# Optimization experiments

Hardware: AMD Instinct MI355X
Metric: run time of the kernel (lower is better)

Reference implementation:

```python
import jax, jax.numpy as jnp
import numpy as np

NHEAD = 8
LAYER_NAMES = ('self', 'cross', 'self', 'cross')
EPS = 1e-6


def ln(x, g, b, eps=1e-5):
    m = jnp.mean(x, -1, keepdims=True)
    v = jnp.mean((x - m) ** 2, -1, keepdims=True)
    return (x - m) * jax.lax.rsqrt(v + eps) * g + b


def linear_attention(q, k, v, q_mask, kv_mask):
    # q: [N, L, H, D], k/v: [N, S, H, D]; LoFTR LinearAttention (elu+1 feature map)
    Q = jax.nn.elu(q) + 1.0
    K = jax.nn.elu(k) + 1.0
    if q_mask is not None:
        Q = Q * q_mask[:, :, None, None].astype(Q.dtype)
    if kv_mask is not None:
        mk = kv_mask[:, :, None, None].astype(K.dtype)
        K = K * mk
        v = v * mk
    v_len = v.shape[1]
    v = v / v_len
    KV = jnp.einsum('nshd,nshv->nhdv', K, v)
    Z = 1.0 / (jnp.einsum('nlhd,nhd->nlh', Q, K.sum(1)) + EPS)
    return jnp.einsum('nlhd,nhdv,nlh->nlhv', Q, KV, Z) * v_len


def enc_layer(x, src, q_mask, kv_mask, Wq, Wk, Wv, Wm, W1, W2, g1, b1, g2, b2):
    # x: [N, L, C], src: [N, S, C]
    N, L, C = x.shape
    S = src.shape[1]
    H, D = NHEAD, C // NHEAD
    q = (x @ Wq).reshape(N, L, H, D)
    k = (src @ Wk).reshape(N, S, H, D)
    v = (src @ Wv).reshape(N, S, H, D)
    msg = linear_attention(q, k, v, q_mask, kv_mask).reshape(N, L, C)
    msg = ln(msg @ Wm, g1, b1)
    msg = ln(jnp.tanh(jnp.concatenate([x, msg], axis=-1) @ W1) @ W2, g2, b2)
    return x + msg


def sample_descriptors(kp, fmap, s):
    # kp: [B, L, K, 2] (x, y) raw-image pixel coords; fmap: [B, C, H, W]; s: stride
    B, C, H, W = fmap.shape
    k = kp - s / 2 + 0.5
    denom = jnp.array([W * s - s / 2 - 0.5, H * s - s / 2 - 0.5], dtype=kp.dtype)
    k = (k / denom) * 2.0 - 1.0  # normalized [-1, 1]
    px = (k[..., 0] + 1.0) * 0.5 * (W - 1)  # align_corners=True grid_sample
    py = (k[..., 1] + 1.0) * 0.5 * (H - 1)
    x0 = jnp.floor(px)
    y0 = jnp.floor(py)
    wx = (px - x0)[..., None]
    wy = (py - y0)[..., None]
    x0i = jnp.clip(x0, 0, W - 1).astype(jnp.int32)
    x1i = jnp.clip(x0 + 1, 0, W - 1).astype(jnp.int32)
    y0i = jnp.clip(y0, 0, H - 1).astype(jnp.int32)
    y1i = jnp.clip(y0 + 1, 0, H - 1).astype(jnp.int32)
    fm = jnp.transpose(fmap, (0, 2, 3, 1))  # [B, H, W, C]
    bidx = jnp.arange(B)[:, None, None]
    g00 = fm[bidx, y0i, x0i]
    g01 = fm[bidx, y0i, x1i]
    g10 = fm[bidx, y1i, x0i]
    g11 = fm[bidx, y1i, x1i]
    out = (1 - wy) * ((1 - wx) * g00 + wx * g01) + wy * ((1 - wx) * g10 + wx * g11)
    # SuperPoint-style L2 normalization of sampled descriptors
    out = out / (jnp.linalg.norm(out, axis=-1, keepdims=True) + 1e-8)
    return out  # [B, L, K, C]


def geo_transformer(feat0, feat1, kp0_cross, kp1_cross, mask_self0, mask_self1,
                    mask_cross0, mask_cross1, Wq, Wk, Wv, Wm, W1, W2, g1, b1, g2, b2,
                    h0, w0, h1, w1, scale):
    B, L0, C = feat0.shape
    L1 = feat1.shape[1]
    K = kp0_cross.shape[2]
    for i, name in enumerate(LAYER_NAMES):
        p = (Wq[i], Wk[i], Wv[i], Wm[i], W1[i], W2[i], g1[i], b1[i], g2[i], b2[i])
        if name == 'self':
            # source = masked subset of x == full source with kv-mask (v_length cancels)
            feat0 = enc_layer(feat0, feat0, None, mask_self0, *p)
            feat1 = enc_layer(feat1, feat1, None, mask_self1, *p)
        else:
            fmap0 = jnp.transpose(feat0.reshape(B, h0, w0, C), (0, 3, 1, 2))
            fmap1 = jnp.transpose(feat1.reshape(B, h1, w1, C), (0, 3, 1, 2))
            f0c = sample_descriptors(kp0_cross, fmap0, scale)  # [B, L1, K, C]
            f1c = sample_descriptors(kp1_cross, fmap1, scale)  # [B, L0, K, C]
            x0 = feat0.reshape(B * L0, 1, C)
            x1 = feat1.reshape(B * L1, 1, C)
            nf0 = enc_layer(x0, f1c.reshape(B * L0, K, C), None,
                            mask_cross1.reshape(B * L0, K), *p)
            nf1 = enc_layer(x1, f0c.reshape(B * L1, K, C), None,
                            mask_cross0.reshape(B * L1, K), *p)
            feat0 = nf0.reshape(B, L0, C)
            feat1 = nf1.reshape(B, L1, C)
    return feat0, feat1


def setup_inputs() -> dict:
    key = jax.random.key(0)
    B, H0, W0, C, K, S, NL = 2, 64, 64, 256, 9, 8, 4
    L = H0 * W0
    ks = jax.random.split(key, 16)
    std = (2.0 / (C + C)) ** 0.5
    std2 = (2.0 / (2 * C + 2 * C)) ** 0.5
    std3 = (2.0 / (2 * C + C)) ** 0.5
    kp0 = jnp.stack([
        jax.random.uniform(ks[2], (B, L, K)) * (W0 * S),
        jax.random.uniform(ks[3], (B, L, K)) * (H0 * S)], axis=-1)
    kp1 = jnp.stack([
        jax.random.uniform(ks[4], (B, L, K)) * (W0 * S),
        jax.random.uniform(ks[5], (B, L, K)) * (H0 * S)], axis=-1)
    return {
        'feat0': jax.random.normal(ks[0], (B, L, C), jnp.float32),
        'feat1': jax.random.normal(ks[1], (B, L, C), jnp.float32),
        'kp0_cross': kp0.astype(jnp.float32),
        'kp1_cross': kp1.astype(jnp.float32),
        'mask_self0': jax.random.bernoulli(ks[6], 0.9, (B, L)),
        'mask_self1': jax.random.bernoulli(ks[7], 0.9, (B, L)),
        'mask_cross0': jax.random.bernoulli(ks[8], 0.8, (B, L, K)),
        'mask_cross1': jax.random.bernoulli(ks[9], 0.8, (B, L, K)),
        'Wq': jax.random.normal(ks[10], (NL, C, C), jnp.float32) * std,
        'Wk': jax.random.normal(ks[11], (NL, C, C), jnp.float32) * std,
        'Wv': jax.random.normal(ks[12], (NL, C, C), jnp.float32) * std,
        'Wm': jax.random.normal(ks[13], (NL, C, C), jnp.float32) * std,
        'W1': jax.random.normal(ks[14], (NL, 2 * C, 2 * C), jnp.float32) * std2,
        'W2': jax.random.normal(ks[15], (NL, 2 * C, C), jnp.float32) * std3,
        'g1': jnp.ones((NL, C), jnp.float32),
        'b1': jnp.zeros((NL, C), jnp.float32),
        'g2': jnp.ones((NL, C), jnp.float32),
        'b2': jnp.zeros((NL, C), jnp.float32),
        'h0': H0, 'w0': W0, 'h1': H0, 'w1': W0, 'scale': S,
    }


def reference(feat0, feat1, kp0_cross, kp1_cross, mask_self0, mask_self1,
              mask_cross0, mask_cross1, Wq, Wk, Wv, Wm, W1, W2, g1, b1, g2, b2,
              h0, w0, h1, w1, scale):
    return geo_transformer(feat0, feat1, kp0_cross, kp1_cross, mask_self0, mask_self1,
                           mask_cross0, mask_cross1, Wq, Wk, Wv, Wm, W1, W2,
                           g1, b1, g2, b2, h0, w0, h1, w1, scale)
```

## Files before the change

kernel.cpp:

```cpp
#include <hip/hip_runtime.h>
#include <cstddef>


#define NROWS 16384

typedef unsigned short ushort_t;
typedef __attribute__((ext_vector_type(8))) short short8;
typedef __attribute__((ext_vector_type(4))) float f32x4;
typedef __attribute__((ext_vector_type(4))) unsigned short ushort4_t;
typedef __attribute__((ext_vector_type(8))) unsigned short ushort8_t;

__device__ __forceinline__ float b2f(unsigned short u) {
    union { unsigned int i; float f; } v; v.i = (unsigned int)u << 16; return v.f;
}
__device__ __forceinline__ unsigned short f2b(float x) {
    union { float f; unsigned int i; } v; v.f = x;
    unsigned int r = v.i + 0x7fffu + ((v.i >> 16) & 1u);
    return (unsigned short)(r >> 16);
}
__device__ __forceinline__ float elu1(float x) {
    return x > 0.f ? x + 1.f : __expf(x);
}

#define ASYNC_COPY16(gptr, lptr) \
    __builtin_amdgcn_global_load_lds((const __attribute__((address_space(1))) void*)(gptr), \
                                     (__attribute__((address_space(3))) void*)(lptr), 16, 0, 0)

template<int ACT>
__global__ __launch_bounds__(256) void gemm_bf16_kernel(
    const ushort_t* __restrict__ A0, const ushort_t* __restrict__ A1, int ksplit,
    int lda0, int lda1, const ushort_t* __restrict__ Wt, int ldw,
    ushort_t* __restrict__ C, int ldc, int Kd)
{
    __shared__ ushort_t As[128 * 64];
    __shared__ ushort_t Bs[128 * 64];

    int tid = threadIdx.x;
    int m0 = blockIdx.y * 128;
    int n0 = blockIdx.x * 128;
    int lane = tid & 63, w = tid >> 6;
    int wrow = w >> 1, wcol = w & 1;
    int quad = lane >> 4, l16 = lane & 15;

    f32x4 acc[4][4];
    #pragma unroll
    for (int i = 0; i < 4; i++)
        #pragma unroll
        for (int j = 0; j < 4; j++) acc[i][j] = (f32x4){0.f, 0.f, 0.f, 0.f};

    for (int kb = 0; kb < Kd; kb += 64) {
        const ushort_t* Ab; int lda, kc;
        if (kb < ksplit) { Ab = A0; lda = lda0; kc = kb; }
        else             { Ab = A1; lda = lda1; kc = kb - ksplit; }

        #pragma unroll
        for (int q = 0; q < 4; q++) {
            int s = q * 256 + tid;
            int kk = s >> 9, p = s & 511;
            int row = p >> 2, c4 = p & 3;
            ASYNC_COPY16(Ab + (size_t)(m0 + row) * lda + kc + kk * 32 + c4 * 8,
                         (char*)As + s * 16);
        }
        #pragma unroll
        for (int q = 0; q < 4; q++) {
            int s = q * 256 + tid;
            int kk = s >> 9, p = s & 511;
            int row = p >> 2, c4 = p & 3;
            ASYNC_COPY16(Wt + (size_t)(n0 + row) * ldw + kb + kk * 32 + c4 * 8,
                         (char*)Bs + s * 16);
        }
        __syncthreads();

        #pragma unroll
        for (int kk = 0; kk < 2; kk++) {
            short8 af[4], bf[4];
            #pragma unroll
            for (int mt = 0; mt < 4; mt++)
                af[mt] = *(const short8*)&As[kk * 4096 + (wrow * 64 + mt * 16 + l16) * 32 + quad * 8];
            #pragma unroll
            for (int nt = 0; nt < 4; nt++)
                bf[nt] = *(const short8*)&Bs[kk * 4096 + (wcol * 64 + nt * 16 + l16) * 32 + quad * 8];
            #pragma unroll
            for (int mt = 0; mt < 4; mt++)
                #pragma unroll
                for (int nt = 0; nt < 4; nt++)
                    acc[mt][nt] = __builtin_amdgcn_mfma_f32_16x16x32_bf16(
                        af[mt], bf[nt], acc[mt][nt], 0, 0, 0);
        }
        __syncthreads();
    }

    #pragma unroll
    for (int mt = 0; mt < 4; mt++) {
        int row = m0 + wrow * 64 + mt * 16 + quad * 4;
        #pragma unroll
        for (int nt = 0; nt < 4; nt++) {
            int col = n0 + wcol * 64 + nt * 16 + l16;
            #pragma unroll
            for (int r = 0; r < 4; r++) {
                float v = acc[mt][nt][r];
                if (ACT) v = tanhf(v);
                C[(size_t)(row + r) * ldc + col] = f2b(v);
            }
        }
    }
}

template<int RES>
__global__ __launch_bounds__(256) void gemm_ln_kernel(
    const ushort_t* __restrict__ A, int lda,
    const ushort_t* __restrict__ Wt, int ldw, int Kd,
    const float* __restrict__ g, const float* __restrict__ bp,
    ushort_t* __restrict__ OutBf,
    const float* __restrict__ Xin, float* __restrict__ Xout)
{
    __shared__ ushort_t As[32 * 64];
    __shared__ ushort_t Bs[256 * 64];
    __shared__ float rsum[4][32];
    __shared__ float rsq[4][32];

    int tid = threadIdx.x;
    int m0 = blockIdx.x * 32;
    int lane = tid & 63, w = tid >> 6;
    int quad = lane >> 4, l16 = lane & 15;

    f32x4 acc[2][4];
    #pragma unroll
    for (int i = 0; i < 2; i++)
        #pragma unroll
        for (int j = 0; j < 4; j++) acc[i][j] = (f32x4){0.f, 0.f, 0.f, 0.f};

    for (int kb = 0; kb < Kd; kb += 64) {
        {
            int s = tid;
            int kk = s >> 7, p = s & 127;
            int row = p >> 2, c4 = p & 3;
            ASYNC_COPY16(A + (size_t)(m0 + row) * lda + kb + kk * 32 + c4 * 8,
                         (char*)As + s * 16);
        }
        #pragma unroll
        for (int q = 0; q < 8; q++) {
            int s = q * 256 + tid;
            int kk = s >> 10, p = s & 1023;
            int row = p >> 2, c4 = p & 3;
            ASYNC_COPY16(Wt + (size_t)(row) * ldw + kb + kk * 32 + c4 * 8,
                         (char*)Bs + s * 16);
        }
        __syncthreads();

        #pragma unroll
        for (int kk = 0; kk < 2; kk++) {
            short8 af[2], bf[4];
            #pragma unroll
            for (int mt = 0; mt < 2; mt++)
                af[mt] = *(const short8*)&As[kk * 1024 + (mt * 16 + l16) * 32 + quad * 8];
            #pragma unroll
            for (int nt = 0; nt < 4; nt++)
                bf[nt] = *(const short8*)&Bs[kk * 8192 + (w * 64 + nt * 16 + l16) * 32 + quad * 8];
            #pragma unroll
            for (int mt = 0; mt < 2; mt++)
                #pragma unroll
                for (int nt = 0; nt < 4; nt++)
                    acc[mt][nt] = __builtin_amdgcn_mfma_f32_16x16x32_bf16(
                        af[mt], bf[nt], acc[mt][nt], 0, 0, 0);
        }
        __syncthreads();
    }

    #pragma unroll
    for (int mt = 0; mt < 2; mt++)
        #pragma unroll
        for (int r = 0; r < 4; r++) {
            float s = 0.f, q = 0.f;
            #pragma unroll
            for (int nt = 0; nt < 4; nt++) {
                float v = acc[mt][nt][r];
                s += v; q += v * v;
            }
            #pragma unroll
            for (int off = 1; off < 16; off <<= 1) {
                s += __shfl_xor(s, off, 64);
                q += __shfl_xor(q, off, 64);
            }
            if (l16 == 0) {
                rsum[w][mt * 16 + quad * 4 + r] = s;
                rsq[w][mt * 16 + quad * 4 + r]  = q;
            }
        }
    __syncthreads();

    #pragma unroll
    for (int mt = 0; mt < 2; mt++) {
        #pragma unroll
        for (int r = 0; r < 4; r++) {
            int rl = mt * 16 + quad * 4 + r;
            float s = rsum[0][rl] + rsum[1][rl] + rsum[2][rl] + rsum[3][rl];
            float q = rsq[0][rl] + rsq[1][rl] + rsq[2][rl] + rsq[3][rl];
            float m = s * (1.f / 256.f);
            float var = q * (1.f / 256.f) - m * m;
            float rs = rsqrtf(var + 1e-5f);
            size_t row = (size_t)(m0 + rl);
            #pragma unroll
            for (int nt = 0; nt < 4; nt++) {
                int col = w * 64 + nt * 16 + l16;
                float y = (acc[mt][nt][r] - m) * rs * g[col] + bp[col];
                if (RES) {
                    float xn = Xin[row * 256 + col] + y;
                    Xout[row * 256 + col] = xn;
                    OutBf[row * 256 + col] = f2b(xn);
                } else {
                    OutBf[row * 256 + col] = f2b(y);
                }
            }
        }
    }
}

__global__ __launch_bounds__(256) void wprep_kernel(
    const float* __restrict__ Wq, const float* __restrict__ Wk,
    const float* __restrict__ Wv, const float* __restrict__ Wm,
    const float* __restrict__ W1, const float* __restrict__ W2,
    ushort_t* __restrict__ Wqkvt, ushort_t* __restrict__ Wmt,
    ushort_t* __restrict__ W1t, ushort_t* __restrict__ W2t)
{
    int t = blockIdx.x;
    int layer = t / 640, r = t % 640;
    const float* src; ushort_t* dst;
    int ldsrc, lddst, tn, tk;
    if (r < 192) {
        int grp = r / 64, rr = r % 64; tn = rr / 8; tk = rr % 8;
        src = (grp == 0 ? Wq : grp == 1 ? Wk : Wv) + (size_t)layer * 65536;
        ldsrc = 256;
        dst = Wqkvt + (size_t)layer * 196608 + (size_t)grp * 65536;
        lddst = 256;
    } else if (r < 256) {
        int rr = r - 192; tn = rr / 8; tk = rr % 8;
        src = Wm + (size_t)layer * 65536; ldsrc = 256;
        dst = Wmt + (size_t)layer * 65536; lddst = 256;
    } else if (r < 512) {
        int rr = r - 256; tn = rr / 16; tk = rr % 16;
        src = W1 + (size_t)layer * 262144; ldsrc = 512;
        dst = W1t + (size_t)layer * 262144; lddst = 512;
    } else {
        int rr = r - 512; tn = rr / 16; tk = rr % 16;
        src = W2 + (size_t)layer * 131072; ldsrc = 256;
        dst = W2t + (size_t)layer * 131072; lddst = 512;
    }
    int n0 = tn * 32, k0 = tk * 32;
    __shared__ float tileS[32][33];
    int j = threadIdx.x & 31, i0 = threadIdx.x >> 5;
    #pragma unroll
    for (int p = 0; p < 4; p++) {
        int i = i0 + p * 8;
        tileS[i][j] = src[(size_t)(k0 + i) * ldsrc + n0 + j];
    }
    __syncthreads();
    #pragma unroll
    for (int p = 0; p < 4; p++) {
        int i = i0 + p * 8;
        dst[(size_t)(n0 + i) * lddst + k0 + j] = f2b(tileS[j][i]);
    }
}

__global__ __launch_bounds__(256) void init_kernel(
    const float* __restrict__ f0, const float* __restrict__ f1,
    float* __restrict__ X, ushort_t* __restrict__ Xbf)
{
    int idx = blockIdx.x * 256 + threadIdx.x;
    size_t e = (size_t)idx * 4;
    float4 v = (e < 2097152) ? *(const float4*)&f0[e] : *(const float4*)&f1[e - 2097152];
    *(float4*)&X[e] = v;
    ushort4_t u = { f2b(v.x), f2b(v.y), f2b(v.z), f2b(v.w) };
    *(ushort4_t*)&Xbf[e] = u;
}

__global__ __launch_bounds__(256) void kv_reduce_kernel(
    const ushort_t* __restrict__ QKV,
    const int* __restrict__ mask0, const int* __restrict__ mask1,
    float* __restrict__ KV, float* __restrict__ Ksum)
{
    int g = blockIdx.y;
    int t = g >> 4, b = (g >> 3) & 1, h = g & 7;
    const int* mask = t ? mask1 : mask0;
    int rowbase = t * 8192 + b * 4096;
    int s_begin = blockIdx.x * 256;

    __shared__ float sK[32][32];
    __shared__ float sV[32][32];

    int tid = threadIdx.x;
    int e  = tid & 31;
    int dq = tid >> 5;

    float acc[4] = {0.f, 0.f, 0.f, 0.f};
    float ks[4]  = {0.f, 0.f, 0.f, 0.f};

    for (int s0 = s_begin; s0 < s_begin + 256; s0 += 32) {
        #pragma unroll
        for (int q = 0; q < 2; q++) {
            int idx = tid + q * 256;
            int rl = idx >> 4;
            int part = idx & 15;
            int s = s0 + rl;
            size_t row = (size_t)(rowbase + s);
            float m = mask[b * 4096 + s] ? 1.f : 0.f;
            if (part < 8) {
                ushort4_t u = *(const ushort4_t*)&QKV[row * 768 + 256 + h * 32 + part * 4];
                float4 f = { elu1(b2f(u.x)) * m, elu1(b2f(u.y)) * m,
                             elu1(b2f(u.z)) * m, elu1(b2f(u.w)) * m };
                *(float4*)&sK[rl][part * 4] = f;
            } else {
                ushort4_t u = *(const ushort4_t*)&QKV[row * 768 + 512 + h * 32 + (part - 8) * 4];
                float4 f = { b2f(u.x) * m, b2f(u.y) * m, b2f(u.z) * m, b2f(u.w) * m };
                *(float4*)&sV[rl][(part - 8) * 4] = f;
            }
        }
        __syncthreads();

        #pragma unroll
        for (int s = 0; s < 32; s++) {
            float4 kq = *(const float4*)&sK[s][dq * 4];
            float vv = sV[s][e];
            acc[0] += kq.x * vv;
            acc[1] += kq.y * vv;
            acc[2] += kq.z * vv;
            acc[3] += kq.w * vv;
            ks[0] += kq.x; ks[1] += kq.y; ks[2] += kq.z; ks[3] += kq.w;
        }
        __syncthreads();
    }

    #pragma unroll
    for (int j = 0; j < 4; j++)
        atomicAdd(&KV[(size_t)g * 1024 + (dq * 4 + j) * 32 + e], acc[j]);
    if (e == 0) {
        #pragma unroll
        for (int j = 0; j < 4; j++)
            atomicAdd(&Ksum[g * 32 + dq * 4 + j], ks[j]);
    }
}

__global__ __launch_bounds__(256) void attn_apply_kernel(
    const ushort_t* __restrict__ QKV, const float* __restrict__ KV,
    const float* __restrict__ Ksum, ushort_t* __restrict__ MSG)
{
    int row = blockIdx.x;
    int t = row >> 13, bb = (row >> 12) & 1;
    int gb = (t * 2 + bb) * 8;
    int c = threadIdx.x, h = c >> 5, e = c & 31;
    int g = gb + h;

    __shared__ float sQ[256];
    float qf = elu1(b2f(QKV[(size_t)row * 768 + c]));
    sQ[c] = qf;
    __syncthreads();

    float p = qf * Ksum[g * 32 + e];
    #pragma unroll
    for (int off = 16; off; off >>= 1) p += __shfl_xor(p, off, 32);
    float Z = 1.f / (p + 1e-6f);

    float acc = 0.f;
    #pragma unroll
    for (int d = 0; d < 32; d++)
        acc += sQ[h * 32 + d] * KV[(size_t)g * 1024 + d * 32 + e];

    MSG[(size_t)row * 256 + c] = f2b(acc * Z);
}

__global__ __launch_bounds__(256) void gram_kernel(
    const ushort_t* __restrict__ Xbf, float* __restrict__ Gm)
{
    int a = blockIdx.x * 4 + (threadIdx.x >> 6);
    int lane = threadIdx.x & 63;
    int img = a / 4225;
    int rr = a - img * 4225;
    int ay = rr / 65, ax = rr - ay * 65;
    int xa = ax > 0 ? ax - 1 : 0;
    int xb = ax < 64 ? ax : 63;
    if (ax == 0) xb = 0;
    int ya = ay > 0 ? ay - 1 : 0;
    int yb = ay < 64 ? ay : 63;
    if (ay == 0) yb = 0;

    size_t rbase = (size_t)img * 4096;
    size_t r0 = (rbase + ya * 64 + xa) * 256;
    size_t r1 = (rbase + ya * 64 + xb) * 256;
    size_t r2 = (rbase + yb * 64 + xa) * 256;
    size_t r3 = (rbase + yb * 64 + xb) * 256;

    int c4 = lane * 4;
    ushort4_t u0 = *(const ushort4_t*)&Xbf[r0 + c4];
    ushort4_t u1 = *(const ushort4_t*)&Xbf[r1 + c4];
    ushort4_t u2 = *(const ushort4_t*)&Xbf[r2 + c4];
    ushort4_t u3 = *(const ushort4_t*)&Xbf[r3 + c4];

    float p[10] = {0,0,0,0,0,0,0,0,0,0};
    #pragma unroll
    for (int j = 0; j < 4; j++) {
        float f0 = b2f(u0[j]), f1 = b2f(u1[j]), f2 = b2f(u2[j]), f3 = b2f(u3[j]);
        p[0] += f0 * f0; p[1] += f0 * f1; p[2] += f0 * f2; p[3] += f0 * f3;
        p[4] += f1 * f1; p[5] += f1 * f2; p[6] += f1 * f3;
        p[7] += f2 * f2; p[8] += f2 * f3; p[9] += f3 * f3;
    }
    #pragma unroll
    for (int k = 0; k < 10; k++)
        #pragma unroll
        for (int off = 32; off; off >>= 1) p[k] += __shfl_xor(p[k], off, 64);

    if (lane == 0) {
        #pragma unroll
        for (int k = 0; k < 10; k++) Gm[(size_t)a * 10 + k] = p[k];
    }
}

__global__ __launch_bounds__(256) void cross_fused_kernel(
    const ushort_t* __restrict__ QKV, const float* __restrict__ Gm,
    const float* __restrict__ kp0, const float* __restrict__ kp1,
    const int* __restrict__ maskc0, const int* __restrict__ maskc1,
    ushort_t* __restrict__ MSG)
{
    int wv = threadIdx.x >> 6;
    int lane = threadIdx.x & 63;
    int half = lane >> 5;
    int l32 = lane & 31;
    int row = blockIdx.x * 4 + wv;

    int t = row >> 13;
    int bl = row & 8191;
    int ts = 1 - t;
    const float* kp = ts ? kp1 : kp0;
    const int* mask = (t == 0) ? maskc1 : maskc0;
    int img = ts * 2 + (bl >> 12);
    size_t rb = (size_t)img * 4096;
    const float* Gimg = Gm + (size_t)img * 42250;

    int c8 = l32 * 8;

    ushort8_t qu = *(const ushort8_t*)&QKV[(size_t)row * 768 + c8];
    float qf[8];
    #pragma unroll
    for (int j = 0; j < 8; j++) qf[j] = elu1(b2f(qu[j]));

    float zsum = 0.f;
    float acc[8] = {0,0,0,0,0,0,0,0};

    for (int s9 = half; s9 < 9; s9 += 2) {
        int r = bl * 9 + s9;
        bool mk = mask[r] != 0;
        if (mk) {
            float xx = kp[(size_t)r * 2 + 0];
            float yy = kp[(size_t)r * 2 + 1];
            float px = (xx - 3.5f) * (63.f / 507.5f);
            float py = (yy - 3.5f) * (63.f / 507.5f);
            float fx = floorf(px), fy = floorf(py);
            float wx = px - fx, wy = py - fy;
            int ix = (int)fx, iy = (int)fy;
            int xa = ix > 0 ? ix : 0;
            int xb = ix + 1 > 0 ? (ix + 1 < 63 ? ix + 1 : 63) : 0;
            int ya = iy > 0 ? iy : 0;
            int yb = iy + 1 > 0 ? (iy + 1 < 63 ? iy + 1 : 63) : 0;

            float w0 = (1.f - wy) * (1.f - wx);
            float w1 = (1.f - wy) * wx;
            float w2 = wy * (1.f - wx);
            float w3 = wy * wx;

            const float* G = &Gimg[(size_t)((iy + 1) * 65 + (ix + 1)) * 10];
            float g00 = G[0], g01 = G[1], g02 = G[2], g03 = G[3], g11 = G[4];
            float g12 = G[5], g13 = G[6], g22 = G[7], g23 = G[8], g33 = G[9];
            float ss = w0 * w0 * g00 + w1 * w1 * g11 + w2 * w2 * g22 + w3 * w3 * g33
                     + 2.f * (w0 * w1 * g01 + w0 * w2 * g02 + w0 * w3 * g03
                            + w1 * w2 * g12 + w1 * w3 * g13 + w2 * w3 * g23);
            float inv = 1.f / (sqrtf(ss) + 1e-8f);
            float u0 = w0 * inv, u1 = w1 * inv, u2 = w2 * inv, u3 = w3 * inv;

            size_t s00 = (rb + ya * 64 + xa) * 768;
            size_t s01 = (rb + ya * 64 + xb) * 768;
            size_t s10 = (rb + yb * 64 + xa) * 768;
            size_t s11 = (rb + yb * 64 + xb) * 768;

            ushort8_t k00 = *(const ushort8_t*)&QKV[s00 + 256 + c8];
            ushort8_t k01 = *(const ushort8_t*)&QKV[s01 + 256 + c8];
            ushort8_t k10 = *(const ushort8_t*)&QKV[s10 + 256 + c8];
            ushort8_t k11 = *(const ushort8_t*)&QKV[s11 + 256 + c8];
            ushort8_t v00 = *(const ushort8_t*)&QKV[s00 + 512 + c8];
            ushort8_t v01 = *(const ushort8_t*)&QKV[s01 + 512 + c8];
            ushort8_t v10 = *(const ushort8_t*)&QKV[s10 + 512 + c8];
            ushort8_t v11 = *(const ushort8_t*)&QKV[s11 + 512 + c8];

            float vc[8];
            float p = 0.f;
            #pragma unroll
            for (int j = 0; j < 8; j++) {
                float kc = u0 * b2f(k00[j]) + u1 * b2f(k01[j])
                         + u2 * b2f(k10[j]) + u3 * b2f(k11[j]);
                vc[j] = u0 * b2f(v00[j]) + u1 * b2f(v01[j])
                      + u2 * b2f(v10[j]) + u3 * b2f(v11[j]);
                p += qf[j] * elu1(kc);
            }
            p += __shfl_xor(p, 1, 64);
            p += __shfl_xor(p, 2, 64);

            zsum += p;
            #pragma unroll
            for (int j = 0; j < 8; j++) acc[j] += p * vc[j];
        }
    }

    zsum += __shfl_xor(zsum, 32, 64);
    #pragma unroll
    for (int j = 0; j < 8; j++) acc[j] += __shfl_xor(acc[j], 32, 64);

    if (half == 0) {
        float Z = 1.f / (zsum + 1e-6f);
        ushort8_t o;
        #pragma unroll
        for (int j = 0; j < 8; j++) o[j] = f2b(acc[j] * Z);
        *(ushort8_t*)&MSG[(size_t)row * 256 + c8] = o;
    }
}


extern "C" void kernel_launch(void* const* d_in, const int* in_sizes, int n_in,
                              void* d_out, int out_size, void* d_ws, size_t ws_size,
                              hipStream_t stream)
{
    const float* feat0 = (const float*)d_in[0];
    const float* feat1 = (const float*)d_in[1];
    const float* kp0 = (const float*)d_in[2];
    const float* kp1 = (const float*)d_in[3];
    const int* ms0 = (const int*)d_in[4];
    const int* ms1 = (const int*)d_in[5];
    const int* mc0 = (const int*)d_in[6];
    const int* mc1 = (const int*)d_in[7];
    const float* Wq = (const float*)d_in[8];
    const float* Wk = (const float*)d_in[9];
    const float* Wv = (const float*)d_in[10];
    const float* Wm = (const float*)d_in[11];
    const float* W1 = (const float*)d_in[12];
    const float* W2 = (const float*)d_in[13];
    const float* g1 = (const float*)d_in[14];
    const float* b1 = (const float*)d_in[15];
    const float* g2 = (const float*)d_in[16];
    const float* b2 = (const float*)d_in[17];

    char* p = (char*)d_ws;
    float*    X     = (float*)p;            p += 16777216;
    ushort_t* Xbf   = (ushort_t*)p;         p += 8388608;
    ushort_t* QKV   = (ushort_t*)p;         p += 25165824;
    ushort_t* MSG   = (ushort_t*)p;         p += 8388608;
    ushort_t* T     = (ushort_t*)p;         p += 16777216;
    ushort_t* L1bf  = (ushort_t*)p;         p += 8388608;
    float*    KVb   = (float*)p;            p += 131072;
    float*    KSb   = (float*)p;            p += 4096;
    float*    Gm    = (float*)p;            p += 679936;
    ushort_t* Wqkvt = (ushort_t*)p;         p += 1572864;
    ushort_t* Wmt   = (ushort_t*)p;         p += 524288;
    ushort_t* W1t   = (ushort_t*)p;         p += 2097152;
    ushort_t* W2t   = (ushort_t*)p;         p += 1048576;

    init_kernel<<<4096, 256, 0, stream>>>(feat0, feat1, X, Xbf);
    wprep_kernel<<<2560, 256, 0, stream>>>(Wq, Wk, Wv, Wm, W1, W2, Wqkvt, Wmt, W1t, W2t);

    auto gemm = [&](const ushort_t* A0, const ushort_t* A1, int ksplit, int lda0, int lda1,
                    const ushort_t* Wtp, int ldw, ushort_t* Cp, int ldc, int N, int Kd, int act) {
        dim3 grid(N / 128, NROWS / 128);
        if (act)
            gemm_bf16_kernel<1><<<grid, 256, 0, stream>>>(A0, A1, ksplit, lda0, lda1, Wtp, ldw, Cp, ldc, Kd);
        else
            gemm_bf16_kernel<0><<<grid, 256, 0, stream>>>(A0, A1, ksplit, lda0, lda1, Wtp, ldw, Cp, ldc, Kd);
    };

    for (int i = 0; i < 4; i++) {
        const ushort_t* Wqkvt_l = Wqkvt + (size_t)i * 196608;
        const ushort_t* Wmt_l   = Wmt   + (size_t)i * 65536;
        const ushort_t* W1t_l   = W1t   + (size_t)i * 262144;
        const ushort_t* W2t_l   = W2t   + (size_t)i * 131072;
        const float* g1_l = g1 + (size_t)i * 256;
        const float* b1_l = b1 + (size_t)i * 256;
        const float* g2_l = g2 + (size_t)i * 256;
        const float* b2_l = b2 + (size_t)i * 256;
        bool is_self = (i == 0 || i == 2);

        gemm(Xbf, nullptr, 1 << 30, 256, 0, Wqkvt_l, 256, QKV, 768, 768, 256, 0);

        if (is_self) {
            hipMemsetAsync(KVb, 0, 33792 * 4, stream);
            kv_reduce_kernel<<<dim3(16, 32), 256, 0, stream>>>(QKV, ms0, ms1, KVb, KSb);
            attn_apply_kernel<<<NROWS, 256, 0, stream>>>(QKV, KVb, KSb, MSG);
        } else {
            gram_kernel<<<4225, 256, 0, stream>>>(Xbf, Gm);
            cross_fused_kernel<<<NROWS / 4, 256, 0, stream>>>(QKV, Gm, kp0, kp1, mc0, mc1, MSG);
        }

        gemm_ln_kernel<0><<<NROWS / 32, 256, 0, stream>>>(
            MSG, 256, Wmt_l, 256, 256, g1_l, b1_l, L1bf, nullptr, nullptr);
        gemm(Xbf, L1bf, 256, 256, 256, W1t_l, 512, T, 512, 512, 512, 1);
        float* Xout = (i == 3) ? (float*)d_out : X;
        gemm_ln_kernel<1><<<NROWS / 32, 256, 0, stream>>>(
            T, 512, W2t_l, 512, 512, g2_l, b2_l, Xbf, X, Xout);
    }
}
```

Measured before the change: 638.6 us.

## Fuse W1 tanh GEMM and W2 GEMM+LayerNorm+residual into one MLP kernel

Replaces the separate W1 GEMM (with tanh) writing the T intermediate and the W2 GEMM+LN+residual kernel with a single kernel per 32-row block. The tanh output is kept in a swizzled LDS tile instead of going through global memory. This removes a 16MB intermediate write and read plus one launch per layer. The cost is that each 32-row block re-streams the full W1 and W2 weights, which means more weight traffic and lower MFMA reuse per block, with only 512 blocks and a large LDS footprint limiting occupancy.

```diff
diff --git a/kernel.cpp b/kernel.cpp
--- a/kernel.cpp
+++ b/kernel.cpp
@@ -26,10 +26,9 @@
     __builtin_amdgcn_global_load_lds((const __attribute__((address_space(1))) void*)(gptr), \
                                      (__attribute__((address_space(3))) void*)(lptr), 16, 0, 0)
 
-template<int ACT>
 __global__ __launch_bounds__(256) void gemm_bf16_kernel(
-    const ushort_t* __restrict__ A0, const ushort_t* __restrict__ A1, int ksplit,
-    int lda0, int lda1, const ushort_t* __restrict__ Wt, int ldw,
+    const ushort_t* __restrict__ A0, int lda0,
+    const ushort_t* __restrict__ Wt, int ldw,
     ushort_t* __restrict__ C, int ldc, int Kd)
 {
     __shared__ ushort_t As[128 * 64];
@@ -49,16 +48,12 @@
         for (int j = 0; j < 4; j++) acc[i][j] = (f32x4){0.f, 0.f, 0.f, 0.f};
 
     for (int kb = 0; kb < Kd; kb += 64) {
-        const ushort_t* Ab; int lda, kc;
-        if (kb < ksplit) { Ab = A0; lda = lda0; kc = kb; }
-        else             { Ab = A1; lda = lda1; kc = kb - ksplit; }
-
         #pragma unroll
         for (int q = 0; q < 4; q++) {
             int s = q * 256 + tid;
             int kk = s >> 9, p = s & 511;
             int row = p >> 2, c4 = p & 3;
-            ASYNC_COPY16(Ab + (size_t)(m0 + row) * lda + kc + kk * 32 + c4 * 8,
+            ASYNC_COPY16(A0 + (size_t)(m0 + row) * lda0 + kb + kk * 32 + c4 * 8,
                          (char*)As + s * 16);
         }
         #pragma unroll
@@ -97,22 +92,17 @@
         for (int nt = 0; nt < 4; nt++) {
             int col = n0 + wcol * 64 + nt * 16 + l16;
             #pragma unroll
-            for (int r = 0; r < 4; r++) {
-                float v = acc[mt][nt][r];
-                if (ACT) v = tanhf(v);
-                C[(size_t)(row + r) * ldc + col] = f2b(v);
-            }
-        }
-    }
-}
-
-template<int RES>
+            for (int r = 0; r < 4; r++)
+                C[(size_t)(row + r) * ldc + col] = f2b(acc[mt][nt][r]);
+        }
+    }
+}
+
 __global__ __launch_bounds__(256) void gemm_ln_kernel(
     const ushort_t* __restrict__ A, int lda,
     const ushort_t* __restrict__ Wt, int ldw, int Kd,
     const float* __restrict__ g, const float* __restrict__ bp,
-    ushort_t* __restrict__ OutBf,
-    const float* __restrict__ Xin, float* __restrict__ Xout)
+    ushort_t* __restrict__ OutBf)
 {
     __shared__ ushort_t As[32 * 64];
     __shared__ ushort_t Bs[256 * 64];
@@ -204,14 +194,177 @@
             for (int nt = 0; nt < 4; nt++) {
                 int col = w * 64 + nt * 16 + l16;
                 float y = (acc[mt][nt][r] - m) * rs * g[col] + bp[col];
-                if (RES) {
+                OutBf[row * 256 + col] = f2b(y);
+            }
+        }
+    }
+}
+
+__global__ __launch_bounds__(256) void mlp_fused_kernel(
+    const ushort_t* __restrict__ Xb, const ushort_t* __restrict__ L1,
+    const ushort_t* __restrict__ W1t, const ushort_t* __restrict__ W2t,
+    const float* __restrict__ g, const float* __restrict__ bp,
+    ushort_t* __restrict__ XbfOut, const float* __restrict__ Xin,
+    float* __restrict__ Xout)
+{
+    __shared__ ushort_t Tt[32 * 512];
+    __shared__ char buf[20480];
+
+    ushort_t* As  = (ushort_t*)buf;
+    ushort_t* Bs  = (ushort_t*)(buf + 4096);
+    ushort_t* Bs2 = (ushort_t*)buf;
+    float* rsum = (float*)buf;
+    float* rsq  = (float*)(buf + 512);
+
+    int tid = threadIdx.x;
+    int m0 = blockIdx.x * 32;
+    int lane = tid & 63, w = tid >> 6;
+    int quad = lane >> 4, l16 = lane & 15;
+
+    for (int np = 0; np < 4; np++) {
+        f32x4 acc[2][2];
+        #pragma unroll
+        for (int i = 0; i < 2; i++)
+            #pragma unroll
+            for (int j = 0; j < 2; j++) acc[i][j] = (f32x4){0.f, 0.f, 0.f, 0.f};
+
+        for (int kb = 0; kb < 512; kb += 64) {
+            const ushort_t* Ab = (kb < 256) ? Xb : L1;
+            int kc = (kb < 256) ? kb : kb - 256;
+            {
+                int s = tid;
+                int kk = s >> 7, p = s & 127;
+                ASYNC_COPY16(Ab + (size_t)(m0 + (p >> 2)) * 256 + kc + kk * 32 + (p & 3) * 8,
+                             (char*)As + s * 16);
+            }
+            #pragma unroll
+            for (int q = 0; q < 4; q++) {
+                int s = q * 256 + tid;
+                int kk = s >> 9, p = s & 511;
+                ASYNC_COPY16(W1t + (size_t)(np * 128 + (p >> 2)) * 512 + kb + kk * 32 + (p & 3) * 8,
+                             (char*)Bs + s * 16);
+            }
+            __syncthreads();
+
+            #pragma unroll
+            for (int kk = 0; kk < 2; kk++) {
+                short8 af[2], bfr[2];
+                #pragma unroll
+                for (int mt = 0; mt < 2; mt++)
+                    af[mt] = *(const short8*)&As[kk * 1024 + (mt * 16 + l16) * 32 + quad * 8];
+                #pragma unroll
+                for (int nt = 0; nt < 2; nt++)
+                    bfr[nt] = *(const short8*)&Bs[kk * 4096 + (w * 32 + nt * 16 + l16) * 32 + quad * 8];
+                #pragma unroll
+                for (int mt = 0; mt < 2; mt++)
+                    #pragma unroll
+                    for (int nt = 0; nt < 2; nt++)
+                        acc[mt][nt] = __builtin_amdgcn_mfma_f32_16x16x32_bf16(
+                            af[mt], bfr[nt], acc[mt][nt], 0, 0, 0);
+            }
+            __syncthreads();
+        }
+
+        #pragma unroll
+        for (int mt = 0; mt < 2; mt++)
+            #pragma unroll
+            for (int nt = 0; nt < 2; nt++)
+                #pragma unroll
+                for (int r = 0; r < 4; r++) {
+                    int trow = mt * 16 + quad * 4 + r;
+                    int col = np * 128 + w * 32 + nt * 16 + l16;
+                    int c8s = (col >> 3) ^ (trow & 7);
+                    Tt[trow * 512 + c8s * 8 + (col & 7)] = f2b(tanhf(acc[mt][nt][r]));
+                }
+    }
+
+    f32x4 acc2[2][2][2];
+    #pragma unroll
+    for (int a = 0; a < 2; a++)
+        #pragma unroll
+        for (int i = 0; i < 2; i++)
+            #pragma unroll
+            for (int j = 0; j < 2; j++) acc2[a][i][j] = (f32x4){0.f, 0.f, 0.f, 0.f};
+
+    for (int pass = 0; pass < 2; pass++) {
+        for (int kb = 0; kb < 512; kb += 64) {
+            #pragma unroll
+            for (int q = 0; q < 4; q++) {
+                int s = q * 256 + tid;
+                int kk = s >> 9, p = s & 511;
+                ASYNC_COPY16(W2t + (size_t)(pass * 128 + (p >> 2)) * 512 + kb + kk * 32 + (p & 3) * 8,
+                             (char*)Bs2 + s * 16);
+            }
+            __syncthreads();
+
+            #pragma unroll
+            for (int kk = 0; kk < 2; kk++) {
+                short8 af[2], bfr[2];
+                #pragma unroll
+                for (int mt = 0; mt < 2; mt++) {
+                    int row = mt * 16 + l16;
+                    int blk = ((kb >> 3) + kk * 4 + quad) ^ (row & 7);
+                    af[mt] = *(const short8*)&Tt[row * 512 + blk * 8];
+                }
+                #pragma unroll
+                for (int nt = 0; nt < 2; nt++)
+                    bfr[nt] = *(const short8*)&Bs2[kk * 4096 + (w * 32 + nt * 16 + l16) * 32 + quad * 8];
+                #pragma unroll
+                for (int mt = 0; mt < 2; mt++)
+                    #pragma unroll
+                    for (int nt = 0; nt < 2; nt++)
+                        acc2[pass][mt][nt] = __builtin_amdgcn_mfma_f32_16x16x32_bf16(
+                            af[mt], bfr[nt], acc2[pass][mt][nt], 0, 0, 0);
+            }
+            __syncthreads();
+        }
+    }
+
+    #pragma unroll
+    for (int mt = 0; mt < 2; mt++)
+        #pragma unroll
+        for (int r = 0; r < 4; r++) {
+            float s = 0.f, q = 0.f;
+            #pragma unroll
+            for (int pass = 0; pass < 2; pass++)
+                #pragma unroll
+                for (int nt = 0; nt < 2; nt++) {
+                    float v = acc2[pass][mt][nt][r];
+                    s += v; q += v * v;
+                }
+            #pragma unroll
+            for (int off = 1; off < 16; off <<= 1) {
+                s += __shfl_xor(s, off, 64);
+                q += __shfl_xor(q, off, 64);
+            }
+            if (l16 == 0) {
+                rsum[w * 32 + mt * 16 + quad * 4 + r] = s;
+                rsq[w * 32 + mt * 16 + quad * 4 + r]  = q;
+            }
+        }
+    __syncthreads();
+
+    #pragma unroll
+    for (int mt = 0; mt < 2; mt++) {
+        #pragma unroll
+        for (int r = 0; r < 4; r++) {
+            int rl = mt * 16 + quad * 4 + r;
+            float s = rsum[rl] + rsum[32 + rl] + rsum[64 + rl] + rsum[96 + rl];
+            float q = rsq[rl] + rsq[32 + rl] + rsq[64 + rl] + rsq[96 + rl];
+            float m = s * (1.f / 256.f);
+            float var = q * (1.f / 256.f) - m * m;
+            float rs = rsqrtf(var + 1e-5f);
+            size_t row = (size_t)(m0 + rl);
+            #pragma unroll
+            for (int pass = 0; pass < 2; pass++)
+                #pragma unroll
+                for (int nt = 0; nt < 2; nt++) {
+                    int col = pass * 128 + w * 32 + nt * 16 + l16;
+                    float y = (acc2[pass][mt][nt][r] - m) * rs * g[col] + bp[col];
                     float xn = Xin[row * 256 + col] + y;
                     Xout[row * 256 + col] = xn;
-                    OutBf[row * 256 + col] = f2b(xn);
-                } else {
-                    OutBf[row * 256 + col] = f2b(y);
+                    XbfOut[row * 256 + col] = f2b(xn);
                 }
-            }
         }
     }
 }
@@ -550,7 +703,6 @@
     ushort_t* Xbf   = (ushort_t*)p;         p += 8388608;
     ushort_t* QKV   = (ushort_t*)p;         p += 25165824;
     ushort_t* MSG   = (ushort_t*)p;         p += 8388608;
-    ushort_t* T     = (ushort_t*)p;         p += 16777216;
     ushort_t* L1bf  = (ushort_t*)p;         p += 8388608;
     float*    KVb   = (float*)p;            p += 131072;
     float*    KSb   = (float*)p;            p += 4096;
@@ -562,15 +714,6 @@
 
     init_kernel<<<4096, 256, 0, stream>>>(feat0, feat1, X, Xbf);
     wprep_kernel<<<2560, 256, 0, stream>>>(Wq, Wk, Wv, Wm, W1, W2, Wqkvt, Wmt, W1t, W2t);
-
-    auto gemm = [&](const ushort_t* A0, const ushort_t* A1, int ksplit, int lda0, int lda1,
-                    const ushort_t* Wtp, int ldw, ushort_t* Cp, int ldc, int N, int Kd, int act) {
-        dim3 grid(N / 128, NROWS / 128);
-        if (act)
-            gemm_bf16_kernel<1><<<grid, 256, 0, stream>>>(A0, A1, ksplit, lda0, lda1, Wtp, ldw, Cp, ldc, Kd);
-        else
-            gemm_bf16_kernel<0><<<grid, 256, 0, stream>>>(A0, A1, ksplit, lda0, lda1, Wtp, ldw, Cp, ldc, Kd);
-    };
 
     for (int i = 0; i < 4; i++) {
         const ushort_t* Wqkvt_l = Wqkvt + (size_t)i * 196608;
@@ -583,7 +726,8 @@
         const float* b2_l = b2 + (size_t)i * 256;
         bool is_self = (i == 0 || i == 2);
 
-        gemm(Xbf, nullptr, 1 << 30, 256, 0, Wqkvt_l, 256, QKV, 768, 768, 256, 0);
+        gemm_bf16_kernel<<<dim3(6, 128), 256, 0, stream>>>(
+            Xbf, 256, Wqkvt_l, 256, QKV, 768, 256);
 
         if (is_self) {
             hipMemsetAsync(KVb, 0, 33792 * 4, stream);
@@ -594,11 +738,11 @@
             cross_fused_kernel<<<NROWS / 4, 256, 0, stream>>>(QKV, Gm, kp0, kp1, mc0, mc1, MSG);
         }
 
-        gemm_ln_kernel<0><<<NROWS / 32, 256, 0, stream>>>(
-            MSG, 256, Wmt_l, 256, 256, g1_l, b1_l, L1bf, nullptr, nullptr);
-        gemm(Xbf, L1bf, 256, 256, 256, W1t_l, 512, T, 512, 512, 512, 1);
+        gemm_ln_kernel<<<NROWS / 32, 256, 0, stream>>>(
+            MSG, 256, Wmt_l, 256, 256, g1_l, b1_l, L1bf);
+
         float* Xout = (i == 3) ? (float*)d_out : X;
-        gemm_ln_kernel<1><<<NROWS / 32, 256, 0, stream>>>(
-            T, 512, W2t_l, 512, 512, g2_l, b2_l, Xbf, X, Xout);
-    }
-}
+        mlp_fused_kernel<<<NROWS / 32, 256, 0, stream>>>(
+            Xbf, L1bf, W1t_l, W2t_l, g2_l, b2_l, Xbf, X, Xout);
+    }
+}
```

After: 613.4 us. 1.04x faster.
